# Kernel optimization log

Hardware: AMD Instinct MI355X
Metric: run time of the kernel (lower is better)

## Reference

```python
import jax, jax.numpy as jnp
import numpy as np

B, D_IN, LAT, C = 16384, 512, 64, 8
HID = [1024, 512, 256]

def _lin(k, fi, fo, scale=0.02):
    k1, k2 = jax.random.split(k)
    return jax.random.normal(k1, (fi, fo), jnp.float32) * scale, jax.random.normal(k2, (fo,), jnp.float32) * scale

def _lin_c(k, fi, fo, scale=0.02):
    k1, k2 = jax.random.split(k)
    return jax.random.normal(k1, (C, fi, fo), jnp.float32) * scale, jax.random.normal(k2, (C, fo), jnp.float32) * scale

def setup_inputs() -> dict:
    key = jax.random.key(0)
    ks = jax.random.split(key, 16)
    x = jax.random.normal(ks[0], (B, D_IN), jnp.float32)
    cluster_labels = jax.random.randint(ks[1], (B,), 0, C, jnp.int32)
    eps = jax.random.normal(ks[2], (B, LAT), jnp.float32)
    # encoder: shared(512->1024), unshared(1024->512), shared(512->256)
    enc_W0, enc_b0 = _lin(ks[3], D_IN, HID[0])
    enc_Wu, enc_bu = _lin_c(ks[4], HID[0], HID[1])
    enc_W2, enc_b2 = _lin(ks[5], HID[1], HID[2])
    # shared latent heads
    mu_W, mu_b = _lin(ks[6], HID[2], LAT)
    lv_W, lv_b = _lin(ks[7], HID[2], LAT)
    # decoder (hidden_dims reversed = [256,512,1024]): unshared(64->256), shared(256->512), unshared(512->1024)
    dec_Wu0, dec_bu0 = _lin_c(ks[8], LAT, HID[2])
    dec_W1, dec_b1 = _lin(ks[9], HID[2], HID[1])
    dec_Wu2, dec_bu2 = _lin_c(ks[10], HID[1], HID[0])
    # per-cluster final layer (1024 -> input_dim), no activation (all-continuous)
    fin_W, fin_b = _lin_c(ks[11], HID[0], D_IN)
    return dict(x=x, cluster_labels=cluster_labels, eps=eps,
                enc_W0=enc_W0, enc_b0=enc_b0, enc_Wu=enc_Wu, enc_bu=enc_bu,
                enc_W2=enc_W2, enc_b2=enc_b2, mu_W=mu_W, mu_b=mu_b,
                lv_W=lv_W, lv_b=lv_b, dec_Wu0=dec_Wu0, dec_bu0=dec_bu0,
                dec_W1=dec_W1, dec_b1=dec_b1, dec_Wu2=dec_Wu2, dec_bu2=dec_bu2,
                fin_W=fin_W, fin_b=fin_b)

def _unshared(h, W, b, labels):
    # per-cluster GEMM then row-wise combine (mask-based dispatch, no row reorder)
    y = jnp.einsum('bi,cio->bco', h, W) + b[None]  # [B, C, out]
    return jnp.take_along_axis(y, labels[:, None, None], axis=1)[:, 0, :]

def reference(x, cluster_labels, eps,
              enc_W0, enc_b0, enc_Wu, enc_bu, enc_W2, enc_b2,
              mu_W, mu_b, lv_W, lv_b,
              dec_Wu0, dec_bu0, dec_W1, dec_b1, dec_Wu2, dec_bu2,
              fin_W, fin_b):
    lbl = cluster_labels.astype(jnp.int32)
    # encoder
    h = jax.nn.relu(x @ enc_W0 + enc_b0)
    h = jax.nn.relu(_unshared(h, enc_Wu, enc_bu, lbl))
    h = jax.nn.relu(h @ enc_W2 + enc_b2)
    mu = h @ mu_W + mu_b
    logvar = h @ lv_W + lv_b
    # reparameterize
    z = mu + jnp.exp(0.5 * logvar) * eps
    # decoder
    h = jax.nn.relu(_unshared(z, dec_Wu0, dec_bu0, lbl))
    h = jax.nn.relu(h @ dec_W1 + dec_b1)
    h = jax.nn.relu(_unshared(h, dec_Wu2, dec_bu2, lbl))
    # per-cluster final output layer (identity activation: all-continuous)
    recon = _unshared(h, fin_W, fin_b, lbl)
    return recon
```

## Files before the change

kernel.cpp:

```cpp
#include <hip/hip_runtime.h>

typedef _Float16 f16;
typedef __attribute__((ext_vector_type(8))) _Float16 f16x8;
typedef __attribute__((ext_vector_type(4))) _Float16 f16x4;
typedef __attribute__((ext_vector_type(4))) float    f32x4;

#define B_ROWS 16384
#define MPAD   17408
#define MTILES 136
#define NBLK   64

typedef __attribute__((address_space(1))) void as1_void;
typedef __attribute__((address_space(3))) void as3_void;

__device__ __forceinline__ void gl_lds16(const void* g, void* l) {
    __builtin_amdgcn_global_load_lds((const as1_void*)g, (as3_void*)l, 16, 0, 0);
}


__global__ __launch_bounds__(256) void k_prep(const int* __restrict__ lbl, int* __restrict__ blockhist,
                                              int* __restrict__ rowmap,
                                              const float* __restrict__ mb_, const float* __restrict__ lb_,
                                              float* __restrict__ bz, f16* __restrict__ zerob) {
    int b = blockIdx.x, t = threadIdx.x;
    int i = b * 256 + t;
    rowmap[i] = -1;
    if (b < NBLK) {
        __shared__ int h[8];
        if (t < 8) h[t] = 0;
        __syncthreads();
        atomicAdd(&h[lbl[i]], 1);
        __syncthreads();
        if (t < 8) blockhist[b * 8 + t] = h[t];
    } else if (b == NBLK) {
        if (t < 64) zerob[t] = (f16)0.f;
        if (t < 64) bz[t] = mb_[t];
        else if (t < 128) bz[t] = lb_[t - 64];
    }
}

__global__ void k_offsets(const int* __restrict__ blockhist, int* offs, int* tilec, int* blockbase) {
    __shared__ int tot[8];
    __shared__ int so[9];
    int t = threadIdx.x;
    if (t < 8) {
        int s = 0;
        for (int b = 0; b < NBLK; ++b) s += blockhist[b * 8 + t];
        tot[t] = s;
    }
    __syncthreads();
    if (t == 0) {
        int o = 0;
        for (int c = 0; c < 8; ++c) { so[c] = o; o += (tot[c] + 127) & ~127; }
        so[8] = o;
        for (int c = 0; c < 9; ++c) offs[c] = so[c];
    }
    __syncthreads();
    if (t < 8) {
        int run = so[t];
        for (int b = 0; b < NBLK; ++b) {
            blockbase[b * 8 + t] = run;
            run += blockhist[b * 8 + t];
        }
    }
    if (t < MTILES) {
        int row = t * 128, c = 7;
        for (int cc = 0; cc < 8; ++cc)
            if (row >= so[cc] && row < so[cc + 1]) c = cc;
        tilec[t] = c;
    }
}

__global__ __launch_bounds__(256) void k_scatter(const int* __restrict__ lbl,
                                                 const int* __restrict__ blockbase,
                                                 int* __restrict__ rowmap) {
    __shared__ int cur[8];
    if (threadIdx.x < 8) cur[threadIdx.x] = blockbase[blockIdx.x * 8 + threadIdx.x];
    __syncthreads();
    int i = blockIdx.x * 256 + threadIdx.x;
    int c = lbl[i];
    int pos = atomicAdd(&cur[c], 1);
    rowmap[pos] = i;
}


struct Seg { const float* s; f16* d; int K, N, b0, nx, ny; long sCS, dCS; };
struct SegTab { Seg g[10]; };

__global__ __launch_bounds__(256) void k_trans(SegTab tab, const float* __restrict__ x, f16* __restrict__ xh) {
    int bid = blockIdx.x;
    if (bid < tab.g[1].b0) {
        int i = bid * 256 + threadIdx.x;
        float4 v = ((const float4*)x)[i];
        f16x4 o = {(f16)v.x, (f16)v.y, (f16)v.z, (f16)v.w};
        ((f16x4*)xh)[i] = o;
        return;
    }
    int s = 9;
    while (bid < tab.g[s].b0) --s;
    Seg sg = tab.g[s];
    int lb = bid - sg.b0;
    int nxy = sg.nx * sg.ny;
    int z = lb / nxy; int r = lb - z * nxy;
    int by = r / sg.nx; int bx = r - by * sg.nx;
    const float* src = sg.s + (size_t)z * sg.sCS;
    f16* dst = sg.d + (size_t)z * sg.dCS;
    int n0 = bx * 32, k0 = by * 32;
    int tx = threadIdx.x & 31, ty = threadIdx.x >> 5;
    __shared__ float t[32][33];
    #pragma unroll
    for (int i = 0; i < 32; i += 8)
        t[ty + i][tx] = src[(size_t)(k0 + ty + i) * sg.N + n0 + tx];
    __syncthreads();
    #pragma unroll
    for (int i = 0; i < 32; i += 8)
        dst[(size_t)(n0 + ty + i) * sg.K + k0 + tx] = (f16)t[tx][ty + i];
}


template<int GATHER, int PERW, int RELU, int EPI>
__global__ __launch_bounds__(256) void gemm_k(
    const f16* __restrict__ A, const f16* __restrict__ Wt,
    const float* __restrict__ bias, f16* __restrict__ Out, float* __restrict__ OutF,
    const float* __restrict__ eps,
    const int* __restrict__ rowmap, const int* __restrict__ tilec,
    const f16* __restrict__ zerobuf, int K, int N)
{
    __shared__ __align__(16) char smem[65536];
    const int tid  = threadIdx.x;
    const int wave = tid >> 6;
    const int lane = tid & 63;

    const int id  = blockIdx.x;
    const int xcd = id & 7;
    const int jj  = id >> 3;
    const int tm  = (jj % 17) * 8 + xcd;
    const int tn  = jj / 17;
    const int r0 = tm * 128, n0 = tn * 128;

    const f16* wb = Wt;
    const float* bb = bias;
    if (PERW) {
        int c = tilec[tm];
        wb += (size_t)c * K * N;
        bb += (size_t)c * N;
    }

    const int srow = tid >> 3;
    const int sg   = tid & 7;
    const int xk16 = (sg ^ (srow & 7)) * 16;
    const size_t rowB = (size_t)K * 2;
    const size_t passB = 32 * rowB;

    const char* pa[4]; size_t stepA[4];
    #pragma unroll
    for (int p = 0; p < 4; ++p) {
        int gr = r0 + p * 32 + srow;
        if (GATHER) {
            int g = rowmap[gr];
            if (g >= 0) { pa[p] = (const char*)(A + (size_t)g * K) + xk16; stepA[p] = 128; }
            else        { pa[p] = (const char*)zerobuf;                    stepA[p] = 0;   }
        } else {
            pa[p] = (const char*)(A + (size_t)gr * K) + xk16; stepA[p] = 128;
        }
    }
    const char* pb = (const char*)(wb + (size_t)(n0 + srow) * K) + xk16;

    const int mb = (wave >> 1) * 64;
    const int nb = (wave & 1) * 64;
    const int quad = lane >> 4;
    const int r16  = lane & 15;
    const int key  = r16 & 7;

    float bv[4];
    #pragma unroll
    for (int j = 0; j < 4; ++j) bv[j] = bb[n0 + nb + j * 16 + r16];

    f32x4 acc[4][4];
    #pragma unroll
    for (int i = 0; i < 4; ++i)
        #pragma unroll
        for (int j = 0; j < 4; ++j)
            acc[i][j] = (f32x4){0.f, 0.f, 0.f, 0.f};

    auto stage = [&](char* dst) {
        #pragma unroll
        for (int p = 0; p < 4; ++p)
            gl_lds16(pa[p], dst + p * 4096 + wave * 1024);
        #pragma unroll
        for (int p = 0; p < 4; ++p)
            gl_lds16(pb + p * passB, dst + 16384 + p * 4096 + wave * 1024);
        #pragma unroll
        for (int p = 0; p < 4; ++p) pa[p] += stepA[p];
        pb += 128;
    };

    auto compute = [&](const char* lA, const char* lB) {
        #pragma unroll
        for (int kk = 0; kk < 2; ++kk) {
            const int off = ((kk * 4 + quad) ^ key) * 16;
            f16x8 af[4], bf[4];
            #pragma unroll
            for (int i = 0; i < 4; ++i)
                af[i] = *(const f16x8*)(lA + (mb + i * 16 + r16) * 128 + off);
            #pragma unroll
            for (int j = 0; j < 4; ++j)
                bf[j] = *(const f16x8*)(lB + (nb + j * 16 + r16) * 128 + off);
            #pragma unroll
            for (int i = 0; i < 4; ++i)
                #pragma unroll
                for (int j = 0; j < 4; ++j)
                    acc[i][j] = __builtin_amdgcn_mfma_f32_16x16x32_f16(af[i], bf[j], acc[i][j], 0, 0, 0);
        }
    };

    const int nk = K >> 6;
    stage(smem);
    __syncthreads();
    int cur = 0;
    for (int kb = 0; kb < nk - 1; ++kb) {
        stage(smem + ((cur ^ 1) << 15));
        compute(smem + (cur << 15), smem + (cur << 15) + 16384);
        __syncthreads();
        cur ^= 1;
    }
    compute(smem + (cur << 15), smem + (cur << 15) + 16384);

    if (EPI == 2) {
        char* cs = smem + ((cur ^ 1) << 15);
        #pragma unroll
        for (int i = 0; i < 4; ++i) {
            #pragma unroll
            for (int r = 0; r < 4; ++r) {
                int lr = mb + i * 16 + quad * 4 + r;
                #pragma unroll
                for (int j = 0; j < 4; ++j) {
                    int lc = nb + j * 16 + r16;
                    float v = acc[i][j][r] + bv[j];
                    *(f16*)(cs + lr * 256 + ((((lc >> 3) ^ (lr & 7))) << 4) + ((lc & 7) << 1)) = (f16)v;
                }
            }
        }
        __syncthreads();
        const int col = tid & 63;
        const int rb  = tid >> 6;
        for (int rr = 0; rr < 32; ++rr) {
            int row = rb * 32 + rr;
            int g = rowmap[r0 + row];
            float e = (g >= 0) ? eps[(size_t)g * 64 + col] : 0.f;
            float mu = (float)*(const f16*)(cs + row * 256 + ((((col >> 3) ^ (row & 7))) << 4) + ((col & 7) << 1));
            int c2 = col + 64;
            float lv = (float)*(const f16*)(cs + row * 256 + ((((c2 >> 3) ^ (row & 7))) << 4) + ((c2 & 7) << 1));
            Out[(size_t)(r0 + row) * 64 + col] = (f16)(mu + expf(0.5f * lv) * e);
        }
        return;
    }

    #pragma unroll
    for (int i = 0; i < 4; ++i) {
        #pragma unroll
        for (int r = 0; r < 4; ++r) {
            int orow = r0 + mb + i * 16 + quad * 4 + r;
            int g = 0;
            if (EPI == 1) g = rowmap[orow];
            #pragma unroll
            for (int j = 0; j < 4; ++j) {
                int ocol = n0 + nb + j * 16 + r16;
                float v = acc[i][j][r] + bv[j];
                if (RELU) v = fmaxf(v, 0.f);
                if (EPI == 1) {
                    if (g >= 0) OutF[(size_t)g * N + ocol] = v;
                } else {
                    Out[(size_t)orow * N + ocol] = (f16)v;
                }
            }
        }
    }
}


extern "C" void kernel_launch(void* const* d_in, const int* in_sizes, int n_in,
                              void* d_out, int out_size, void* d_ws, size_t ws_size,
                              hipStream_t stream) {
    const float* x      = (const float*)d_in[0];
    const int*   lbl    = (const int*)  d_in[1];
    const float* eps    = (const float*)d_in[2];
    const float* enc_W0 = (const float*)d_in[3];
    const float* enc_b0 = (const float*)d_in[4];
    const float* enc_Wu = (const float*)d_in[5];
    const float* enc_bu = (const float*)d_in[6];
    const float* enc_W2 = (const float*)d_in[7];
    const float* enc_b2 = (const float*)d_in[8];
    const float* mu_W   = (const float*)d_in[9];
    const float* mu_b   = (const float*)d_in[10];
    const float* lv_W   = (const float*)d_in[11];
    const float* lv_b   = (const float*)d_in[12];
    const float* dWu0   = (const float*)d_in[13];
    const float* dbu0   = (const float*)d_in[14];
    const float* dW1    = (const float*)d_in[15];
    const float* db1    = (const float*)d_in[16];
    const float* dWu2   = (const float*)d_in[17];
    const float* dbu2   = (const float*)d_in[18];
    const float* finW   = (const float*)d_in[19];
    const float* finb   = (const float*)d_in[20];
    float* out = (float*)d_out;
    (void)in_sizes; (void)n_in; (void)out_size; (void)ws_size;

    char* base = (char*)d_ws;
    size_t off = 0;
    auto alloc = [&](size_t bytes) { char* r = base + off; off = (off + bytes + 255) & ~(size_t)255; return r; };
    f16* xh     = (f16*)alloc((size_t)B_ROWS * 512 * 2);
    f16* buf1   = (f16*)alloc((size_t)MPAD * 1024 * 2);
    f16* buf2   = (f16*)alloc((size_t)MPAD * 512 * 2);
    f16* buf3   = (f16*)alloc((size_t)MPAD * 256 * 2);
    f16* zb     = (f16*)alloc((size_t)MPAD * 64 * 2);
    f16* w0t    = (f16*)alloc(1024ul * 512 * 2);
    f16* wut    = (f16*)alloc(8ul * 512 * 1024 * 2);
    f16* w2t    = (f16*)alloc(256ul * 512 * 2);
    f16* wzt    = (f16*)alloc(128ul * 256 * 2);
    f16* wd0t   = (f16*)alloc(8ul * 256 * 64 * 2);
    f16* wd1t   = (f16*)alloc(512ul * 256 * 2);
    f16* wd2t   = (f16*)alloc(8ul * 1024 * 512 * 2);
    f16* wft    = (f16*)alloc(8ul * 512 * 1024 * 2);
    float* bz   = (float*)alloc(128 * 4);
    int* rowmap = (int*)alloc(MPAD * 4);
    int* blockhist = (int*)alloc(NBLK * 8 * 4);
    int* blockbase = (int*)alloc(NBLK * 8 * 4);
    int* offs   = (int*)alloc(64);
    int* tilec  = (int*)alloc(MTILES * 4);
    f16* zerob  = (f16*)alloc(256);

    k_prep<<<MPAD / 256, 256, 0, stream>>>(lbl, blockhist, rowmap, mu_b, lv_b, bz, zerob);
    k_offsets<<<1, 256, 0, stream>>>(blockhist, offs, tilec, blockbase);
    k_scatter<<<NBLK, 256, 0, stream>>>(lbl, blockbase, rowmap);

    SegTab tab;
    int b0 = B_ROWS * 512 / 4 / 256;
    auto seg = [&](int i, const float* s, f16* d, int K, int N, int nz, long sCS, long dCS) {
        int nx = N / 32, ny = K / 32;
        tab.g[i] = Seg{s, d, K, N, b0, nx, ny, sCS, dCS};
        b0 += nx * ny * nz;
    };
    tab.g[0] = Seg{nullptr, nullptr, 0, 0, 0, 0, 0, 0, 0};
    seg(1, enc_W0, w0t, 512, 1024, 1, 0, 0);
    seg(2, enc_Wu, wut, 1024, 512, 8, 1024l * 512, 512l * 1024);
    seg(3, enc_W2, w2t, 512, 256, 1, 0, 0);
    seg(4, mu_W, wzt, 256, 64, 1, 0, 0);
    seg(5, lv_W, wzt + 64 * 256, 256, 64, 1, 0, 0);
    seg(6, dWu0, wd0t, 64, 256, 8, 64l * 256, 256l * 64);
    seg(7, dW1, wd1t, 256, 512, 1, 0, 0);
    seg(8, dWu2, wd2t, 512, 1024, 8, 512l * 1024, 1024l * 512);
    seg(9, finW, wft, 1024, 512, 8, 1024l * 512, 512l * 1024);
    k_trans<<<b0, 256, 0, stream>>>(tab, x, xh);

    gemm_k<1,0,1,0><<<MTILES * 8, 256, 0, stream>>>(xh,   w0t,  enc_b0, buf1, nullptr, nullptr, rowmap, tilec, zerob, 512, 1024);
    gemm_k<0,1,1,0><<<MTILES * 4, 256, 0, stream>>>(buf1, wut,  enc_bu, buf2, nullptr, nullptr, rowmap, tilec, zerob, 1024, 512);
    gemm_k<0,0,1,0><<<MTILES * 2, 256, 0, stream>>>(buf2, w2t,  enc_b2, buf3, nullptr, nullptr, rowmap, tilec, zerob, 512, 256);
    gemm_k<0,0,0,2><<<MTILES * 1, 256, 0, stream>>>(buf3, wzt,  bz,     zb,   nullptr, eps,     rowmap, tilec, zerob, 256, 128);
    gemm_k<0,1,1,0><<<MTILES * 2, 256, 0, stream>>>(zb,   wd0t, dbu0,   buf3, nullptr, nullptr, rowmap, tilec, zerob, 64, 256);
    gemm_k<0,0,1,0><<<MTILES * 4, 256, 0, stream>>>(buf3, wd1t, db1,    buf2, nullptr, nullptr, rowmap, tilec, zerob, 256, 512);
    gemm_k<0,1,1,0><<<MTILES * 8, 256, 0, stream>>>(buf2, wd2t, dbu2,   buf1, nullptr, nullptr, rowmap, tilec, zerob, 512, 1024);
    gemm_k<0,1,0,1><<<MTILES * 4, 256, 0, stream>>>(buf1, wft,  finb,   nullptr, out,  nullptr, rowmap, tilec, zerob, 1024, 512);
}
```

Measured before the change: 362.6 us.

## Halve GEMM K-tile to raise occupancy and widen transpose/convert kernels

```diff
diff --git a/kernel.cpp b/kernel.cpp
--- a/kernel.cpp
+++ b/kernel.cpp
@@ -89,11 +89,14 @@
 
 __global__ __launch_bounds__(256) void k_trans(SegTab tab, const float* __restrict__ x, f16* __restrict__ xh) {
     int bid = blockIdx.x;
+    int t = threadIdx.x;
     if (bid < tab.g[1].b0) {
-        int i = bid * 256 + threadIdx.x;
-        float4 v = ((const float4*)x)[i];
-        f16x4 o = {(f16)v.x, (f16)v.y, (f16)v.z, (f16)v.w};
-        ((f16x4*)xh)[i] = o;
+        size_t i = (size_t)bid * 256 + t;
+        float4 a = ((const float4*)x)[2 * i];
+        float4 b = ((const float4*)x)[2 * i + 1];
+        f16x8 o = {(f16)a.x, (f16)a.y, (f16)a.z, (f16)a.w,
+                   (f16)b.x, (f16)b.y, (f16)b.z, (f16)b.w};
+        ((f16x8*)xh)[i] = o;
         return;
     }
     int s = 9;
@@ -105,16 +108,24 @@
     int by = r / sg.nx; int bx = r - by * sg.nx;
     const float* src = sg.s + (size_t)z * sg.sCS;
     f16* dst = sg.d + (size_t)z * sg.dCS;
-    int n0 = bx * 32, k0 = by * 32;
-    int tx = threadIdx.x & 31, ty = threadIdx.x >> 5;
-    __shared__ float t[32][33];
-    #pragma unroll
-    for (int i = 0; i < 32; i += 8)
-        t[ty + i][tx] = src[(size_t)(k0 + ty + i) * sg.N + n0 + tx];
-    __syncthreads();
-    #pragma unroll
-    for (int i = 0; i < 32; i += 8)
-        dst[(size_t)(n0 + ty + i) * sg.K + k0 + tx] = (f16)t[tx][ty + i];
+    int n0 = bx * 64, k0 = by * 64;
+    __shared__ float ld[64][64];
+    int cr = t >> 4, cc = (t & 15) * 4;
+    #pragma unroll
+    for (int i = 0; i < 4; ++i) {
+        float4 v = *(const float4*)(src + (size_t)(k0 + cr + 16 * i) * sg.N + n0 + cc);
+        *(float4*)&ld[cr + 16 * i][cc] = v;
+    }
+    __syncthreads();
+    int n = t & 63, gp = t >> 6;
+    #pragma unroll
+    for (int p = 0; p < 2; ++p) {
+        int g = gp + 4 * p;
+        f16x8 o;
+        #pragma unroll
+        for (int j = 0; j < 8; ++j) o[j] = (f16)ld[g * 8 + j][n];
+        *(f16x8*)(dst + (size_t)(n0 + n) * sg.K + k0 + g * 8) = o;
+    }
 }
 
 
@@ -126,7 +137,7 @@
     const int* __restrict__ rowmap, const int* __restrict__ tilec,
     const f16* __restrict__ zerobuf, int K, int N)
 {
-    __shared__ __align__(16) char smem[65536];
+    __shared__ __align__(16) char smem[32768];
     const int tid  = threadIdx.x;
     const int wave = tid >> 6;
     const int lane = tid & 63;
@@ -146,31 +157,31 @@
         bb += (size_t)c * N;
     }
 
-    const int srow = tid >> 3;
-    const int sg   = tid & 7;
-    const int xk16 = (sg ^ (srow & 7)) * 16;
+    const int srow = tid >> 2;
+    const int sg   = tid & 3;
+    const int xk16 = (sg ^ ((srow >> 1) & 3)) * 16;
     const size_t rowB = (size_t)K * 2;
-    const size_t passB = 32 * rowB;
-
-    const char* pa[4]; size_t stepA[4];
-    #pragma unroll
-    for (int p = 0; p < 4; ++p) {
-        int gr = r0 + p * 32 + srow;
+
+    const char* pa[2]; size_t stepA[2];
+    #pragma unroll
+    for (int p = 0; p < 2; ++p) {
+        int gr = r0 + p * 64 + srow;
         if (GATHER) {
             int g = rowmap[gr];
-            if (g >= 0) { pa[p] = (const char*)(A + (size_t)g * K) + xk16; stepA[p] = 128; }
-            else        { pa[p] = (const char*)zerobuf;                    stepA[p] = 0;   }
+            if (g >= 0) { pa[p] = (const char*)(A + (size_t)g * K) + xk16; stepA[p] = 64; }
+            else        { pa[p] = (const char*)zerobuf;                    stepA[p] = 0;  }
         } else {
-            pa[p] = (const char*)(A + (size_t)gr * K) + xk16; stepA[p] = 128;
+            pa[p] = (const char*)(A + (size_t)gr * K) + xk16; stepA[p] = 64;
         }
     }
     const char* pb = (const char*)(wb + (size_t)(n0 + srow) * K) + xk16;
+    const size_t pbOff = 64 * rowB;
 
     const int mb = (wave >> 1) * 64;
     const int nb = (wave & 1) * 64;
     const int quad = lane >> 4;
     const int r16  = lane & 15;
-    const int key  = r16 & 7;
+    const int off  = (quad ^ ((r16 >> 1) & 3)) * 16;
 
     float bv[4];
     #pragma unroll
@@ -184,50 +195,45 @@
             acc[i][j] = (f32x4){0.f, 0.f, 0.f, 0.f};
 
     auto stage = [&](char* dst) {
-        #pragma unroll
-        for (int p = 0; p < 4; ++p)
-            gl_lds16(pa[p], dst + p * 4096 + wave * 1024);
-        #pragma unroll
-        for (int p = 0; p < 4; ++p)
-            gl_lds16(pb + p * passB, dst + 16384 + p * 4096 + wave * 1024);
-        #pragma unroll
-        for (int p = 0; p < 4; ++p) pa[p] += stepA[p];
-        pb += 128;
+        gl_lds16(pa[0], dst        + wave * 1024);
+        gl_lds16(pa[1], dst + 4096 + wave * 1024);
+        gl_lds16(pb,           dst + 8192  + wave * 1024);
+        gl_lds16(pb + pbOff,   dst + 12288 + wave * 1024);
+        pa[0] += stepA[0]; pa[1] += stepA[1];
+        pb += 64;
     };
 
-    auto compute = [&](const char* lA, const char* lB) {
-        #pragma unroll
-        for (int kk = 0; kk < 2; ++kk) {
-            const int off = ((kk * 4 + quad) ^ key) * 16;
-            f16x8 af[4], bf[4];
-            #pragma unroll
-            for (int i = 0; i < 4; ++i)
-                af[i] = *(const f16x8*)(lA + (mb + i * 16 + r16) * 128 + off);
+    auto compute = [&](const char* base) {
+        const char* lA = base;
+        const char* lB = base + 8192;
+        f16x8 af[4], bf[4];
+        #pragma unroll
+        for (int i = 0; i < 4; ++i)
+            af[i] = *(const f16x8*)(lA + (mb + i * 16 + r16) * 64 + off);
+        #pragma unroll
+        for (int j = 0; j < 4; ++j)
+            bf[j] = *(const f16x8*)(lB + (nb + j * 16 + r16) * 64 + off);
+        #pragma unroll
+        for (int i = 0; i < 4; ++i)
             #pragma unroll
             for (int j = 0; j < 4; ++j)
-                bf[j] = *(const f16x8*)(lB + (nb + j * 16 + r16) * 128 + off);
-            #pragma unroll
-            for (int i = 0; i < 4; ++i)
-                #pragma unroll
-                for (int j = 0; j < 4; ++j)
-                    acc[i][j] = __builtin_amdgcn_mfma_f32_16x16x32_f16(af[i], bf[j], acc[i][j], 0, 0, 0);
-        }
+                acc[i][j] = __builtin_amdgcn_mfma_f32_16x16x32_f16(af[i], bf[j], acc[i][j], 0, 0, 0);
     };
 
-    const int nk = K >> 6;
+    const int nk = K >> 5;
     stage(smem);
     __syncthreads();
     int cur = 0;
     for (int kb = 0; kb < nk - 1; ++kb) {
-        stage(smem + ((cur ^ 1) << 15));
-        compute(smem + (cur << 15), smem + (cur << 15) + 16384);
+        stage(smem + ((cur ^ 1) << 14));
+        compute(smem + (cur << 14));
         __syncthreads();
         cur ^= 1;
     }
-    compute(smem + (cur << 15), smem + (cur << 15) + 16384);
+    compute(smem + (cur << 14));
 
     if (EPI == 2) {
-        char* cs = smem + ((cur ^ 1) << 15);
+        __syncthreads();
         #pragma unroll
         for (int i = 0; i < 4; ++i) {
             #pragma unroll
@@ -237,7 +243,7 @@
                 for (int j = 0; j < 4; ++j) {
                     int lc = nb + j * 16 + r16;
                     float v = acc[i][j][r] + bv[j];
-                    *(f16*)(cs + lr * 256 + ((((lc >> 3) ^ (lr & 7))) << 4) + ((lc & 7) << 1)) = (f16)v;
+                    *(f16*)(smem + lr * 256 + ((((lc >> 3) ^ (lr & 7))) << 4) + ((lc & 7) << 1)) = (f16)v;
                 }
             }
         }
@@ -248,9 +254,9 @@
             int row = rb * 32 + rr;
             int g = rowmap[r0 + row];
             float e = (g >= 0) ? eps[(size_t)g * 64 + col] : 0.f;
-            float mu = (float)*(const f16*)(cs + row * 256 + ((((col >> 3) ^ (row & 7))) << 4) + ((col & 7) << 1));
+            float mu = (float)*(const f16*)(smem + row * 256 + ((((col >> 3) ^ (row & 7))) << 4) + ((col & 7) << 1));
             int c2 = col + 64;
-            float lv = (float)*(const f16*)(cs + row * 256 + ((((c2 >> 3) ^ (row & 7))) << 4) + ((c2 & 7) << 1));
+            float lv = (float)*(const f16*)(smem + row * 256 + ((((c2 >> 3) ^ (row & 7))) << 4) + ((c2 & 7) << 1));
             Out[(size_t)(r0 + row) * 64 + col] = (f16)(mu + expf(0.5f * lv) * e);
         }
         return;
@@ -335,9 +341,9 @@
     k_scatter<<<NBLK, 256, 0, stream>>>(lbl, blockbase, rowmap);
 
     SegTab tab;
-    int b0 = B_ROWS * 512 / 4 / 256;
+    int b0 = B_ROWS * 512 / 8 / 256;
     auto seg = [&](int i, const float* s, f16* d, int K, int N, int nz, long sCS, long dCS) {
-        int nx = N / 32, ny = K / 32;
+        int nx = N / 64, ny = K / 64;
         tab.g[i] = Seg{s, d, K, N, b0, nx, ny, sCS, dCS};
         b0 += nx * ny * nz;
     };
```

Result: no change. 363.2 us (+0.2%).

## Widen transpose/convert tiles and use split vmcnt barriers in GEMM pipeline

Applied to the files above, without the earlier changes.

```diff
diff --git a/kernel.cpp b/kernel.cpp
--- a/kernel.cpp
+++ b/kernel.cpp
@@ -89,11 +89,14 @@
 
 __global__ __launch_bounds__(256) void k_trans(SegTab tab, const float* __restrict__ x, f16* __restrict__ xh) {
     int bid = blockIdx.x;
+    int t = threadIdx.x;
     if (bid < tab.g[1].b0) {
-        int i = bid * 256 + threadIdx.x;
-        float4 v = ((const float4*)x)[i];
-        f16x4 o = {(f16)v.x, (f16)v.y, (f16)v.z, (f16)v.w};
-        ((f16x4*)xh)[i] = o;
+        size_t i = (size_t)bid * 256 + t;
+        float4 a = ((const float4*)x)[2 * i];
+        float4 b = ((const float4*)x)[2 * i + 1];
+        f16x8 o = {(f16)a.x, (f16)a.y, (f16)a.z, (f16)a.w,
+                   (f16)b.x, (f16)b.y, (f16)b.z, (f16)b.w};
+        ((f16x8*)xh)[i] = o;
         return;
     }
     int s = 9;
@@ -105,16 +108,28 @@
     int by = r / sg.nx; int bx = r - by * sg.nx;
     const float* src = sg.s + (size_t)z * sg.sCS;
     f16* dst = sg.d + (size_t)z * sg.dCS;
-    int n0 = bx * 32, k0 = by * 32;
-    int tx = threadIdx.x & 31, ty = threadIdx.x >> 5;
-    __shared__ float t[32][33];
-    #pragma unroll
-    for (int i = 0; i < 32; i += 8)
-        t[ty + i][tx] = src[(size_t)(k0 + ty + i) * sg.N + n0 + tx];
+    int n0 = bx * 64, k0 = by * 64;
+    __shared__ float ld[64][64];
+    int cr = t >> 4, cc = (t & 15) * 4;
+    #pragma unroll
+    for (int i = 0; i < 4; ++i) {
+        int rr = cr + 16 * i;
+        float4 v = *(const float4*)(src + (size_t)(k0 + rr) * sg.N + n0 + cc);
+        *(float4*)&ld[rr][(((cc >> 2) ^ (rr & 15)) << 2)] = v;
+    }
     __syncthreads();
     #pragma unroll
-    for (int i = 0; i < 32; i += 8)
-        dst[(size_t)(n0 + ty + i) * sg.K + k0 + tx] = (f16)t[tx][ty + i];
+    for (int p = 0; p < 2; ++p) {
+        int G = p * 256 + t;
+        int n = G >> 3, gg = G & 7;
+        f16x8 o;
+        #pragma unroll
+        for (int j = 0; j < 8; ++j) {
+            int kk = gg * 8 + j;
+            o[j] = (f16)ld[kk][(((n >> 2) ^ (kk & 15)) << 2) | (n & 3)];
+        }
+        *(f16x8*)(dst + (size_t)(n0 + n) * sg.K + k0 + gg * 8) = o;
+    }
 }
 
 
@@ -195,7 +210,9 @@
         pb += 128;
     };
 
-    auto compute = [&](const char* lA, const char* lB) {
+    auto compute = [&](const char* base) {
+        const char* lA = base;
+        const char* lB = base + 16384;
         #pragma unroll
         for (int kk = 0; kk < 2; ++kk) {
             const int off = ((kk * 4 + quad) ^ key) * 16;
@@ -216,18 +233,21 @@
 
     const int nk = K >> 6;
     stage(smem);
-    __syncthreads();
     int cur = 0;
     for (int kb = 0; kb < nk - 1; ++kb) {
         stage(smem + ((cur ^ 1) << 15));
-        compute(smem + (cur << 15), smem + (cur << 15) + 16384);
+        asm volatile("s_waitcnt vmcnt(8)" ::: "memory");
+        __builtin_amdgcn_s_barrier();
+        compute(smem + (cur << 15));
+        __builtin_amdgcn_s_barrier();
+        cur ^= 1;
+    }
+    asm volatile("s_waitcnt vmcnt(0)" ::: "memory");
+    __builtin_amdgcn_s_barrier();
+    compute(smem + (cur << 15));
+
+    if (EPI == 2) {
         __syncthreads();
-        cur ^= 1;
-    }
-    compute(smem + (cur << 15), smem + (cur << 15) + 16384);
-
-    if (EPI == 2) {
-        char* cs = smem + ((cur ^ 1) << 15);
         #pragma unroll
         for (int i = 0; i < 4; ++i) {
             #pragma unroll
@@ -237,7 +257,7 @@
                 for (int j = 0; j < 4; ++j) {
                     int lc = nb + j * 16 + r16;
                     float v = acc[i][j][r] + bv[j];
-                    *(f16*)(cs + lr * 256 + ((((lc >> 3) ^ (lr & 7))) << 4) + ((lc & 7) << 1)) = (f16)v;
+                    *(f16*)(smem + lr * 256 + ((((lc >> 3) ^ (lr & 7))) << 4) + ((lc & 7) << 1)) = (f16)v;
                 }
             }
         }
@@ -248,9 +268,9 @@
             int row = rb * 32 + rr;
             int g = rowmap[r0 + row];
             float e = (g >= 0) ? eps[(size_t)g * 64 + col] : 0.f;
-            float mu = (float)*(const f16*)(cs + row * 256 + ((((col >> 3) ^ (row & 7))) << 4) + ((col & 7) << 1));
+            float mu = (float)*(const f16*)(smem + row * 256 + ((((col >> 3) ^ (row & 7))) << 4) + ((col & 7) << 1));
             int c2 = col + 64;
-            float lv = (float)*(const f16*)(cs + row * 256 + ((((c2 >> 3) ^ (row & 7))) << 4) + ((c2 & 7) << 1));
+            float lv = (float)*(const f16*)(smem + row * 256 + ((((c2 >> 3) ^ (row & 7))) << 4) + ((c2 & 7) << 1));
             Out[(size_t)(r0 + row) * 64 + col] = (f16)(mu + expf(0.5f * lv) * e);
         }
         return;
@@ -335,9 +355,9 @@
     k_scatter<<<NBLK, 256, 0, stream>>>(lbl, blockbase, rowmap);
 
     SegTab tab;
-    int b0 = B_ROWS * 512 / 4 / 256;
+    int b0 = B_ROWS * 512 / 8 / 256;
     auto seg = [&](int i, const float* s, f16* d, int K, int N, int nz, long sCS, long dCS) {
-        int nx = N / 32, ny = K / 32;
+        int nx = N / 64, ny = K / 64;
         tab.g[i] = Seg{s, d, K, N, b0, nx, ny, sCS, dCS};
         b0 += nx * ny * nz;
     };
```

Result: no change. 361.4 us (-0.3%).
